# Performance work log

Hardware: AMD Instinct MI355X
Metric: run time of the kernel (lower is better)

The kernel has to match this reference:

```python
import jax, jax.numpy as jnp
import numpy as np

IN_F, OUT_F = 4096, 4096
TOKENS = 8192


def setup_inputs() -> dict:
    key = jax.random.key(0)
    k = jax.random.split(key, 7)
    return {
        "x": jax.random.normal(k[0], (TOKENS, IN_F), dtype=jnp.float32),
        "weight_mu": jax.random.normal(k[1], (OUT_F, IN_F), dtype=jnp.float32) * 0.02,
        "weight_rho": jax.random.normal(k[2], (OUT_F, IN_F), dtype=jnp.float32) - 4.6,
        "bias_mu": jax.random.normal(k[3], (OUT_F,), dtype=jnp.float32) * 0.02,
        "bias_rho": jax.random.normal(k[4], (OUT_F,), dtype=jnp.float32) - 4.6,
        "eps_w": jax.random.normal(k[5], (OUT_F, IN_F), dtype=jnp.float32),
        "eps_b": jax.random.normal(k[6], (OUT_F,), dtype=jnp.float32),
    }


def reference(x, weight_mu, weight_rho, bias_mu, bias_rho, eps_w, eps_b):
    # Reparameterized sampling: W = mu + softplus(rho) * eps  (use_softplus=True)
    w = weight_mu + jax.nn.softplus(weight_rho) * eps_w      # [out, in]
    b = bias_mu + jax.nn.softplus(bias_rho) * eps_b          # [out]
    # F.linear: y = x @ W^T + b
    return jnp.einsum("ti,oi->to", x, w) + b
```

## Files before the change

### kernel.cpp

```cpp
#include <hip/hip_runtime.h>
#include <hip/hip_bf16.h>

#define TOKENS 8192
#define IN_F   4096
#define OUT_F  4096

typedef __attribute__((ext_vector_type(8))) short bf16x8;
typedef __attribute__((ext_vector_type(4))) float f32x4;

static __device__ __forceinline__ unsigned short f2bf(float f) {
    union { float f; unsigned int u; } v;
    v.f = f;
    unsigned int r = v.u + 0x7fffu + ((v.u >> 16) & 1u);
    return (unsigned short)(r >> 16);
}

static __device__ __forceinline__ float softplus(float x) {
    return log1pf(__expf(x));
}

__global__ void prep_w_kernel(const float* __restrict__ mu,
                              const float* __restrict__ rho,
                              const float* __restrict__ eps,
                              __hip_bfloat16* __restrict__ w) {
    int i = blockIdx.x * 256 + threadIdx.x;
    float4 m4 = ((const float4*)mu)[i];
    float4 r4 = ((const float4*)rho)[i];
    float4 e4 = ((const float4*)eps)[i];
    ushort4 o;
    o.x = f2bf(m4.x + softplus(r4.x) * e4.x);
    o.y = f2bf(m4.y + softplus(r4.y) * e4.y);
    o.z = f2bf(m4.z + softplus(r4.z) * e4.z);
    o.w = f2bf(m4.w + softplus(r4.w) * e4.w);
    ((ushort4*)w)[i] = o;
}

__global__ void conv_x_kernel(const float* __restrict__ x,
                              __hip_bfloat16* __restrict__ xb) {
    int i = blockIdx.x * 256 + threadIdx.x;
    float4 v = ((const float4*)x)[i];
    ushort4 o;
    o.x = f2bf(v.x); o.y = f2bf(v.y); o.z = f2bf(v.z); o.w = f2bf(v.w);
    ((ushort4*)xb)[i] = o;
}

__global__ void prep_b_kernel(const float* __restrict__ bmu,
                              const float* __restrict__ brho,
                              const float* __restrict__ beps,
                              float* __restrict__ b) {
    int i = blockIdx.x * 256 + threadIdx.x;
    b[i] = bmu[i] + softplus(brho[i]) * beps[i];
}

__global__ __launch_bounds__(256) void gemm_bt_kernel(
        const __hip_bfloat16* __restrict__ Xb,
        const __hip_bfloat16* __restrict__ Wb,
        const float* __restrict__ bias,
        float* __restrict__ C) {
    __shared__ __hip_bfloat16 lds_a[128 * 32];
    __shared__ __hip_bfloat16 lds_b[128 * 32];

    const int tid  = threadIdx.x;
    const int lane = tid & 63;
    const int wave = tid >> 6;
    const int K    = IN_F;

    const int rowBase = blockIdx.y * 128;
    const int colBase = blockIdx.x * 128;

    const int srow   = tid >> 2;
    const int schunk = tid & 3;
    const __hip_bfloat16* gA0 = Xb + (size_t)(rowBase + srow) * K + schunk * 8;
    const __hip_bfloat16* gA1 = gA0 + (size_t)64 * K;
    const __hip_bfloat16* gB0 = Wb + (size_t)(colBase + srow) * K + schunk * 8;
    const __hip_bfloat16* gB1 = gB0 + (size_t)64 * K;

    __hip_bfloat16* lA0 = &lds_a[wave * 512 + lane * 8];
    __hip_bfloat16* lA1 = lA0 + 2048;
    __hip_bfloat16* lB0 = &lds_b[wave * 512 + lane * 8];
    __hip_bfloat16* lB1 = lB0 + 2048;

    f32x4 acc[4][4];
#pragma unroll
    for (int i = 0; i < 4; ++i)
#pragma unroll
        for (int j = 0; j < 4; ++j) acc[i][j] = (f32x4){0.f, 0.f, 0.f, 0.f};

    const int wm   = (wave >> 1) * 64;
    const int wn   = (wave & 1) * 64;
    const int fr   = lane & 15;
    const int quad = lane >> 4;

    for (int k0 = 0; k0 < K; k0 += 32) {
        __syncthreads();
        __builtin_amdgcn_global_load_lds(
            (const __attribute__((address_space(1))) void*)(gA0 + k0),
            (__attribute__((address_space(3))) void*)lA0, 16, 0, 0);
        __builtin_amdgcn_global_load_lds(
            (const __attribute__((address_space(1))) void*)(gA1 + k0),
            (__attribute__((address_space(3))) void*)lA1, 16, 0, 0);
        __builtin_amdgcn_global_load_lds(
            (const __attribute__((address_space(1))) void*)(gB0 + k0),
            (__attribute__((address_space(3))) void*)lB0, 16, 0, 0);
        __builtin_amdgcn_global_load_lds(
            (const __attribute__((address_space(1))) void*)(gB1 + k0),
            (__attribute__((address_space(3))) void*)lB1, 16, 0, 0);
        __syncthreads();

        bf16x8 af[4], bfr[4];
#pragma unroll
        for (int mt = 0; mt < 4; ++mt)
            af[mt] = *(const bf16x8*)&lds_a[(wm + mt * 16 + fr) * 32 + quad * 8];
#pragma unroll
        for (int nt = 0; nt < 4; ++nt)
            bfr[nt] = *(const bf16x8*)&lds_b[(wn + nt * 16 + fr) * 32 + quad * 8];

#pragma unroll
        for (int mt = 0; mt < 4; ++mt)
#pragma unroll
            for (int nt = 0; nt < 4; ++nt)
                acc[mt][nt] = __builtin_amdgcn_mfma_f32_16x16x32_bf16(
                    af[mt], bfr[nt], acc[mt][nt], 0, 0, 0);
    }

#pragma unroll
    for (int nt = 0; nt < 4; ++nt) {
        const int col = colBase + wn + nt * 16 + fr;
        const float bv = bias[col];
#pragma unroll
        for (int mt = 0; mt < 4; ++mt) {
            const int row = rowBase + wm + mt * 16 + quad * 4;
#pragma unroll
            for (int r = 0; r < 4; ++r)
                C[(size_t)(row + r) * OUT_F + col] = acc[mt][nt][r] + bv;
        }
    }
}

extern "C" void kernel_launch(void* const* d_in, const int* in_sizes, int n_in,
                              void* d_out, int out_size, void* d_ws, size_t ws_size,
                              hipStream_t stream) {
    const float* x    = (const float*)d_in[0];
    const float* wmu  = (const float*)d_in[1];
    const float* wrho = (const float*)d_in[2];
    const float* bmu  = (const float*)d_in[3];
    const float* brho = (const float*)d_in[4];
    const float* epsw = (const float*)d_in[5];
    const float* epsb = (const float*)d_in[6];
    float* out = (float*)d_out;

    char* ws = (char*)d_ws;
    __hip_bfloat16* xb = (__hip_bfloat16*)ws;
    __hip_bfloat16* wb = (__hip_bfloat16*)(ws + (size_t)TOKENS * IN_F * 2);
    float* bias = (float*)(ws + (size_t)TOKENS * IN_F * 2 + (size_t)OUT_F * IN_F * 2);

    conv_x_kernel<<<(TOKENS * IN_F) / 4 / 256, 256, 0, stream>>>(x, xb);
    prep_w_kernel<<<(OUT_F * IN_F) / 4 / 256, 256, 0, stream>>>(wmu, wrho, epsw, wb);
    prep_b_kernel<<<OUT_F / 256, 256, 0, stream>>>(bmu, brho, epsb, bias);

    dim3 grid(OUT_F / 128, TOKENS / 128);
    gemm_bt_kernel<<<grid, 256, 0, stream>>>(xb, wb, bias, out);
}
```

Measured before the change: 674.6 us.

## Fuse prep kernels and rewrite GEMM as pipelined 256x256 tile kernel

Merges the three preprocessing kernels into one launch and switches softplus to fast intrinsics. Replaces the 128x128 single-buffered GEMM with a 256x256-tile, 512-thread kernel. The new kernel double-buffers K=64 slices in LDS using XOR-swizzled layouts, interleaves global-to-LDS prefetch with MFMA phases and raises wave priority during compute. The aim is to hide load latency, reduce LDS bank conflicts and improve data reuse. In exchange it uses more LDS and registers per block, and the grid has only 512 blocks.

```diff
diff --git a/kernel.cpp b/kernel.cpp
--- a/kernel.cpp
+++ b/kernel.cpp
@@ -4,6 +4,11 @@
 #define TOKENS 8192
 #define IN_F   4096
 #define OUT_F  4096
+
+#define BM 256
+#define BN 256
+#define BK 64
+#define NT (IN_F / BK)
 
 typedef __attribute__((ext_vector_type(8))) short bf16x8;
 typedef __attribute__((ext_vector_type(4))) float f32x4;
@@ -15,124 +20,204 @@
     return (unsigned short)(r >> 16);
 }
 
-static __device__ __forceinline__ float softplus(float x) {
-    return log1pf(__expf(x));
-}
-
-__global__ void prep_w_kernel(const float* __restrict__ mu,
-                              const float* __restrict__ rho,
-                              const float* __restrict__ eps,
-                              __hip_bfloat16* __restrict__ w) {
-    int i = blockIdx.x * 256 + threadIdx.x;
-    float4 m4 = ((const float4*)mu)[i];
-    float4 r4 = ((const float4*)rho)[i];
-    float4 e4 = ((const float4*)eps)[i];
-    ushort4 o;
-    o.x = f2bf(m4.x + softplus(r4.x) * e4.x);
-    o.y = f2bf(m4.y + softplus(r4.y) * e4.y);
-    o.z = f2bf(m4.z + softplus(r4.z) * e4.z);
-    o.w = f2bf(m4.w + softplus(r4.w) * e4.w);
-    ((ushort4*)w)[i] = o;
-}
-
-__global__ void conv_x_kernel(const float* __restrict__ x,
-                              __hip_bfloat16* __restrict__ xb) {
-    int i = blockIdx.x * 256 + threadIdx.x;
-    float4 v = ((const float4*)x)[i];
-    ushort4 o;
-    o.x = f2bf(v.x); o.y = f2bf(v.y); o.z = f2bf(v.z); o.w = f2bf(v.w);
-    ((ushort4*)xb)[i] = o;
-}
-
-__global__ void prep_b_kernel(const float* __restrict__ bmu,
-                              const float* __restrict__ brho,
-                              const float* __restrict__ beps,
-                              float* __restrict__ b) {
-    int i = blockIdx.x * 256 + threadIdx.x;
-    b[i] = bmu[i] + softplus(brho[i]) * beps[i];
-}
-
-__global__ __launch_bounds__(256) void gemm_bt_kernel(
+static __device__ __forceinline__ float softplus_fast(float x) {
+    return __logf(1.0f + __expf(x));
+}
+
+#define XBLK 32768
+#define WBLK 16384
+
+__global__ __launch_bounds__(256) void prep_all_kernel(
+        const float* __restrict__ x,
+        const float* __restrict__ wmu,  const float* __restrict__ wrho,
+        const float* __restrict__ epsw,
+        const float* __restrict__ bmu,  const float* __restrict__ brho,
+        const float* __restrict__ bepsb,
+        __hip_bfloat16* __restrict__ xb, __hip_bfloat16* __restrict__ wb,
+        float* __restrict__ bias) {
+    const int b = blockIdx.x, t = threadIdx.x;
+    if (b < XBLK) {
+        const int i = b * 256 + t;
+        float4 v = ((const float4*)x)[i];
+        ushort4 o;
+        o.x = f2bf(v.x); o.y = f2bf(v.y); o.z = f2bf(v.z); o.w = f2bf(v.w);
+        ((ushort4*)xb)[i] = o;
+    } else if (b < XBLK + WBLK) {
+        const int i = (b - XBLK) * 256 + t;
+        float4 m4 = ((const float4*)wmu)[i];
+        float4 r4 = ((const float4*)wrho)[i];
+        float4 e4 = ((const float4*)epsw)[i];
+        ushort4 o;
+        o.x = f2bf(m4.x + softplus_fast(r4.x) * e4.x);
+        o.y = f2bf(m4.y + softplus_fast(r4.y) * e4.y);
+        o.z = f2bf(m4.z + softplus_fast(r4.z) * e4.z);
+        o.w = f2bf(m4.w + softplus_fast(r4.w) * e4.w);
+        ((ushort4*)wb)[i] = o;
+    } else {
+        const int i = (b - XBLK - WBLK) * 256 + t;
+        float4 m4 = ((const float4*)bmu)[i];
+        float4 r4 = ((const float4*)brho)[i];
+        float4 e4 = ((const float4*)bepsb)[i];
+        float4 o;
+        o.x = m4.x + softplus_fast(r4.x) * e4.x;
+        o.y = m4.y + softplus_fast(r4.y) * e4.y;
+        o.z = m4.z + softplus_fast(r4.z) * e4.z;
+        o.w = m4.w + softplus_fast(r4.w) * e4.w;
+        ((float4*)bias)[i] = o;
+    }
+}
+
+__global__ __launch_bounds__(512, 2) void gemm_256_kernel(
         const __hip_bfloat16* __restrict__ Xb,
         const __hip_bfloat16* __restrict__ Wb,
         const float* __restrict__ bias,
         float* __restrict__ C) {
-    __shared__ __hip_bfloat16 lds_a[128 * 32];
-    __shared__ __hip_bfloat16 lds_b[128 * 32];
+    __shared__ __align__(16) __hip_bfloat16 ldsA[2][2][BM * 32];
+    __shared__ __align__(16) __hip_bfloat16 ldsB[2][2][BN * 32];
 
     const int tid  = threadIdx.x;
     const int lane = tid & 63;
     const int wave = tid >> 6;
-    const int K    = IN_F;
-
-    const int rowBase = blockIdx.y * 128;
-    const int colBase = blockIdx.x * 128;
-
-    const int srow   = tid >> 2;
-    const int schunk = tid & 3;
-    const __hip_bfloat16* gA0 = Xb + (size_t)(rowBase + srow) * K + schunk * 8;
-    const __hip_bfloat16* gA1 = gA0 + (size_t)64 * K;
-    const __hip_bfloat16* gB0 = Wb + (size_t)(colBase + srow) * K + schunk * 8;
-    const __hip_bfloat16* gB1 = gB0 + (size_t)64 * K;
-
-    __hip_bfloat16* lA0 = &lds_a[wave * 512 + lane * 8];
-    __hip_bfloat16* lA1 = lA0 + 2048;
-    __hip_bfloat16* lB0 = &lds_b[wave * 512 + lane * 8];
-    __hip_bfloat16* lB1 = lB0 + 2048;
-
-    f32x4 acc[4][4];
-#pragma unroll
-    for (int i = 0; i < 4; ++i)
-#pragma unroll
-        for (int j = 0; j < 4; ++j) acc[i][j] = (f32x4){0.f, 0.f, 0.f, 0.f};
-
-    const int wm   = (wave >> 1) * 64;
-    const int wn   = (wave & 1) * 64;
+    const int wm   = wave >> 2;
+    const int wn   = wave & 3;
     const int fr   = lane & 15;
     const int quad = lane >> 4;
 
-    for (int k0 = 0; k0 < K; k0 += 32) {
-        __syncthreads();
-        __builtin_amdgcn_global_load_lds(
-            (const __attribute__((address_space(1))) void*)(gA0 + k0),
-            (__attribute__((address_space(3))) void*)lA0, 16, 0, 0);
-        __builtin_amdgcn_global_load_lds(
-            (const __attribute__((address_space(1))) void*)(gA1 + k0),
-            (__attribute__((address_space(3))) void*)lA1, 16, 0, 0);
-        __builtin_amdgcn_global_load_lds(
-            (const __attribute__((address_space(1))) void*)(gB0 + k0),
-            (__attribute__((address_space(3))) void*)lB0, 16, 0, 0);
-        __builtin_amdgcn_global_load_lds(
-            (const __attribute__((address_space(1))) void*)(gB1 + k0),
-            (__attribute__((address_space(3))) void*)lB1, 16, 0, 0);
-        __syncthreads();
-
-        bf16x8 af[4], bfr[4];
-#pragma unroll
-        for (int mt = 0; mt < 4; ++mt)
-            af[mt] = *(const bf16x8*)&lds_a[(wm + mt * 16 + fr) * 32 + quad * 8];
-#pragma unroll
-        for (int nt = 0; nt < 4; ++nt)
-            bfr[nt] = *(const bf16x8*)&lds_b[(wn + nt * 16 + fr) * 32 + quad * 8];
-
-#pragma unroll
-        for (int mt = 0; mt < 4; ++mt)
-#pragma unroll
-            for (int nt = 0; nt < 4; ++nt)
-                acc[mt][nt] = __builtin_amdgcn_mfma_f32_16x16x32_bf16(
-                    af[mt], bfr[nt], acc[mt][nt], 0, 0, 0);
+    const int rowBase = blockIdx.y * BM;
+    const int colBase = blockIdx.x * BN;
+
+    const int sRow = tid >> 2;
+    const int sCol = ((tid & 3) ^ ((tid >> 3) & 3)) * 8;
+    const __hip_bfloat16* gA = Xb + (size_t)(rowBase + sRow) * IN_F + sCol;
+    const __hip_bfloat16* gB = Wb + (size_t)(colBase + sRow) * IN_F + sCol;
+    const int dstE = tid * 8;
+
+    const int chunk = quad ^ ((fr >> 1) & 3);
+    const int aOffE = wm * 4096 + fr * 32 + chunk * 8;
+    const int bOffE = wn * 2048 + fr * 32 + chunk * 8;
+
+    auto stageA = [&](int slot, int kh, int kt) {
+        const __hip_bfloat16* src = gA + (size_t)kt * BK + (size_t)kh * 32;
+        __hip_bfloat16* dst = &ldsA[slot][kh][dstE];
+        __builtin_amdgcn_global_load_lds(
+            (const __attribute__((address_space(1))) void*)src,
+            (__attribute__((address_space(3))) void*)dst, 16, 0, 0);
+        __builtin_amdgcn_global_load_lds(
+            (const __attribute__((address_space(1))) void*)(src + (size_t)128 * IN_F),
+            (__attribute__((address_space(3))) void*)(dst + 4096), 16, 0, 0);
+    };
+    auto stageB = [&](int slot, int kh, int kt) {
+        const __hip_bfloat16* src = gB + (size_t)kt * BK + (size_t)kh * 32;
+        __hip_bfloat16* dst = &ldsB[slot][kh][dstE];
+        __builtin_amdgcn_global_load_lds(
+            (const __attribute__((address_space(1))) void*)src,
+            (__attribute__((address_space(3))) void*)dst, 16, 0, 0);
+        __builtin_amdgcn_global_load_lds(
+            (const __attribute__((address_space(1))) void*)(src + (size_t)128 * IN_F),
+            (__attribute__((address_space(3))) void*)(dst + 4096), 16, 0, 0);
+    };
+
+    f32x4 acc[8][4];
+#pragma unroll
+    for (int m = 0; m < 8; ++m)
+#pragma unroll
+        for (int n = 0; n < 4; ++n) acc[m][n] = (f32x4){0.f, 0.f, 0.f, 0.f};
+
+    stageA(0, 0, 0);
+    stageB(0, 0, 0);
+    stageA(0, 1, 0);
+    stageB(0, 1, 0);
+    stageA(1, 0, 1);
+    asm volatile("s_waitcnt vmcnt(6)" ::: "memory");
+    __builtin_amdgcn_s_barrier();
+    __builtin_amdgcn_sched_barrier(0);
+
+    bf16x8 aR[4], bR[4];
+
+    for (int t = 0; t < NT; ++t) {
+        const int cs = t & 1, ns = cs ^ 1;
+        const int t1 = (t + 1 < NT) ? (t + 1) : (NT - 1);
+        const int t2 = (t + 2 < NT) ? (t + 2) : (NT - 1);
+        const __hip_bfloat16* A0 = &ldsA[cs][0][0];
+        const __hip_bfloat16* A1 = &ldsA[cs][1][0];
+        const __hip_bfloat16* B0 = &ldsB[cs][0][0];
+        const __hip_bfloat16* B1 = &ldsB[cs][1][0];
+
+#pragma unroll
+        for (int m = 0; m < 4; ++m) aR[m] = *(const bf16x8*)(A0 + aOffE + m * 512);
+#pragma unroll
+        for (int n = 0; n < 4; ++n) bR[n] = *(const bf16x8*)(B0 + bOffE + n * 512);
+        stageB(ns, 0, t1);
+        __builtin_amdgcn_s_barrier();
+        asm volatile("s_waitcnt lgkmcnt(0)" ::: "memory");
+        __builtin_amdgcn_s_setprio(1);
+#pragma unroll
+        for (int n = 0; n < 4; ++n)
+#pragma unroll
+            for (int m = 0; m < 4; ++m)
+                acc[m][n] = __builtin_amdgcn_mfma_f32_16x16x32_bf16(aR[m], bR[n], acc[m][n], 0, 0, 0);
+        __builtin_amdgcn_s_setprio(0);
+        __builtin_amdgcn_s_barrier();
+
+#pragma unroll
+        for (int m = 0; m < 4; ++m) aR[m] = *(const bf16x8*)(A0 + aOffE + (m + 4) * 512);
+        stageA(ns, 1, t1);
+        __builtin_amdgcn_s_barrier();
+        asm volatile("s_waitcnt lgkmcnt(0)" ::: "memory");
+        __builtin_amdgcn_s_setprio(1);
+#pragma unroll
+        for (int n = 0; n < 4; ++n)
+#pragma unroll
+            for (int m = 0; m < 4; ++m)
+                acc[m + 4][n] = __builtin_amdgcn_mfma_f32_16x16x32_bf16(aR[m], bR[n], acc[m + 4][n], 0, 0, 0);
+        __builtin_amdgcn_s_setprio(0);
+        asm volatile("s_waitcnt vmcnt(6)" ::: "memory");
+        __builtin_amdgcn_s_barrier();
+        __builtin_amdgcn_sched_barrier(0);
+
+#pragma unroll
+        for (int m = 0; m < 4; ++m) aR[m] = *(const bf16x8*)(A1 + aOffE + m * 512);
+#pragma unroll
+        for (int n = 0; n < 4; ++n) bR[n] = *(const bf16x8*)(B1 + bOffE + n * 512);
+        stageB(ns, 1, t1);
+        __builtin_amdgcn_s_barrier();
+        asm volatile("s_waitcnt lgkmcnt(0)" ::: "memory");
+        __builtin_amdgcn_s_setprio(1);
+#pragma unroll
+        for (int n = 0; n < 4; ++n)
+#pragma unroll
+            for (int m = 0; m < 4; ++m)
+                acc[m][n] = __builtin_amdgcn_mfma_f32_16x16x32_bf16(aR[m], bR[n], acc[m][n], 0, 0, 0);
+        __builtin_amdgcn_s_setprio(0);
+        __builtin_amdgcn_s_barrier();
+
+#pragma unroll
+        for (int m = 0; m < 4; ++m) aR[m] = *(const bf16x8*)(A1 + aOffE + (m + 4) * 512);
+        stageA(cs, 0, t2);
+        __builtin_amdgcn_s_barrier();
+        asm volatile("s_waitcnt lgkmcnt(0)" ::: "memory");
+        __builtin_amdgcn_s_setprio(1);
+#pragma unroll
+        for (int n = 0; n < 4; ++n)
+#pragma unroll
+            for (int m = 0; m < 4; ++m)
+                acc[m + 4][n] = __builtin_amdgcn_mfma_f32_16x16x32_bf16(aR[m], bR[n], acc[m + 4][n], 0, 0, 0);
+        __builtin_amdgcn_s_setprio(0);
+        asm volatile("s_waitcnt vmcnt(6)" ::: "memory");
+        __builtin_amdgcn_s_barrier();
+        __builtin_amdgcn_sched_barrier(0);
     }
 
 #pragma unroll
-    for (int nt = 0; nt < 4; ++nt) {
-        const int col = colBase + wn + nt * 16 + fr;
+    for (int n = 0; n < 4; ++n) {
+        const int col = colBase + wn * 64 + n * 16 + fr;
         const float bv = bias[col];
 #pragma unroll
-        for (int mt = 0; mt < 4; ++mt) {
-            const int row = rowBase + wm + mt * 16 + quad * 4;
+        for (int m = 0; m < 8; ++m) {
+            const int row = rowBase + wm * 128 + m * 16 + quad * 4;
 #pragma unroll
             for (int r = 0; r < 4; ++r)
-                C[(size_t)(row + r) * OUT_F + col] = acc[mt][nt][r] + bv;
+                C[(size_t)(row + r) * OUT_F + col] = acc[m][n][r] + bv;
         }
     }
 }
@@ -154,10 +239,9 @@
     __hip_bfloat16* wb = (__hip_bfloat16*)(ws + (size_t)TOKENS * IN_F * 2);
     float* bias = (float*)(ws + (size_t)TOKENS * IN_F * 2 + (size_t)OUT_F * IN_F * 2);
 
-    conv_x_kernel<<<(TOKENS * IN_F) / 4 / 256, 256, 0, stream>>>(x, xb);
-    prep_w_kernel<<<(OUT_F * IN_F) / 4 / 256, 256, 0, stream>>>(wmu, wrho, epsw, wb);
-    prep_b_kernel<<<OUT_F / 256, 256, 0, stream>>>(bmu, brho, epsb, bias);
-
-    dim3 grid(OUT_F / 128, TOKENS / 128);
-    gemm_bt_kernel<<<grid, 256, 0, stream>>>(xb, wb, bias, out);
-}
+    prep_all_kernel<<<XBLK + WBLK + 4, 256, 0, stream>>>(
+        x, wmu, wrho, epsw, bmu, brho, epsb, xb, wb, bias);
+
+    dim3 grid(OUT_F / BN, TOKENS / BM);
+    gemm_256_kernel<<<grid, 512, 0, stream>>>(xb, wb, bias, out);
+}
```

New measurement: 596.1 us. -11.6%, faster.
